# Kernel optimization log

Measured on AMD Instinct MI355X. Metric: run time of the kernel, lower is better.

The kernel has to match this reference:

```python
import jax, jax.numpy as jnp
from jax import lax
import numpy as np

L = 6            # layer_number
CHEB2 = 4        # chebyshev_number ** 2
C = 4 * CHEB2    # per-block channel size = 16
G = 2 ** L       # final block grid = 64 (freq_len / leftover)


def _pool_avg2(y):
    # AvgPool2d kernel=2 stride=2 (dims always divisible here)
    B, Ch, H, W = y.shape
    return y.reshape(B, Ch, H // 2, 2, W // 2, 2).mean(axis=(3, 5))


def _wrap_pad1(y):
    # period_padding by 1 on bottom/right (circular)
    return jnp.pad(y, ((0, 0), (0, 0), (0, 1), (0, 1)), mode='wrap')


def _conv(x, w, groups=1):
    return lax.conv_general_dilated(x, w, (1, 1), 'VALID', feature_group_count=groups)


def _forward(x, W0, b0, Wr, br, Wft, bft):
    B = x.shape[0]
    z0 = jnp.zeros_like(x)
    # split: real input -> (Re+, Re-, Im+=0, Im-=0) per channel (in_channel=1)
    y = jnp.concatenate([jax.nn.relu(x), jax.nn.relu(-x), z0, z0], axis=1)  # [B,4,64,64]
    # layer 0: kernel (w_h,w_w)=(2,2), 4 -> 4*4*cheb^2 = 64
    y = _conv(y, W0) + b0[None, :, None, None]  # [B,64,63,63]
    y = jax.nn.relu(y)
    y = _pool_avg2(_wrap_pad1(y))               # [B,64,32,32] = 2^(L-1) grid
    # recursion layers: per-block 2x2 conv C -> 4C, batched as grouped conv
    for lyr in range(1, L):
        g = 2 ** lyr
        nb = g * g
        z = _conv(y, Wr[lyr - 1], groups=nb) + br[lyr - 1][None, :, None, None]
        s = z.shape[-1]                          # 2^(L-lyr) - 1
        # grouped-conv channel order [A_y, A_x, y_loc, x_loc, C] ->
        # target block index 2^(lyr+1)*(2*A_y+y_loc) + (2*A_x+x_loc):
        z = z.reshape(B, g, g, 2, 2, C, s, s).transpose(0, 1, 3, 2, 4, 5, 6, 7)
        z = z.reshape(B, nb * 4 * C, s, s)
        z = jax.nn.relu(z)
        y = _pool_avg2(_wrap_pad1(z))            # spatial halves -> 2^(L-lyr-1)
    # FT layer: 4^L blocks, 1x1 conv C -> 4*leftover^2 = 4, spatial is 1x1
    v = y.reshape(B, G * G, C)
    f = jnp.einsum('bnc,noc->bno', v, Wft) + bft[None]  # [B,4096,4]
    f = f.reshape(B, G, G, 4)                            # (ky, kx) frequency grid
    real = f[..., 0] - f[..., 1]
    imag = f[..., 2] - f[..., 3]
    return jnp.stack([real, imag], axis=1)               # [B,2,64,64]


def setup_inputs() -> dict:
    key = jax.random.key(0)
    ks = jax.random.split(key, 16)
    sc = 0.1
    inp = {
        'x':  jax.random.normal(ks[0], (256, 1, 64, 64), jnp.float32),
        'W0': sc * jax.random.normal(ks[1], (64, 4, 2, 2), jnp.float32),
        'b0': sc * jax.random.normal(ks[2], (64,), jnp.float32),
        'Wft': sc * jax.random.normal(ks[3], (4096, 4, 16), jnp.float32),
        'bft': sc * jax.random.normal(ks[4], (4096, 4), jnp.float32),
    }
    for lyr in range(1, L):
        nb = 4 ** lyr
        inp[f'W{lyr}'] = sc * jax.random.normal(ks[4 + 2 * lyr - 1], (nb * 4 * C, C, 2, 2), jnp.float32)
        inp[f'b{lyr}'] = sc * jax.random.normal(ks[4 + 2 * lyr], (nb * 4 * C,), jnp.float32)
    return inp


def reference(x, W0, b0, W1, b1, W2, b2, W3, b3, W4, b4, W5, b5, Wft, bft):
    Wr = (W1, W2, W3, W4, W5)
    br = (b1, b2, b3, b4, b5)
    return _forward(x, W0, b0, Wr, br, Wft, bft)
```

## Files before the change

kernel.cpp:

```cpp
#include <hip/hip_runtime.h>
#include <hip/hip_bf16.h>


typedef __attribute__((ext_vector_type(4))) float f32x4;
typedef __attribute__((ext_vector_type(8))) short s16x8;

__device__ __forceinline__ short f2bf(float f) {
  union { float f; unsigned u; } v; v.f = f;
  unsigned r = v.u + 0x7fff + ((v.u >> 16) & 1);
  return (short)(r >> 16);
}
__device__ __forceinline__ float bf2f(short s) {
  union { unsigned u; float f; } v; v.u = ((unsigned)(unsigned short)s) << 16;
  return v.f;
}
constexpr int ilog2c(int v) { return v <= 1 ? 0 : 1 + ilog2c(v / 2); }

__global__ __launch_bounds__(256) void k_layer0(
    const float* __restrict__ x, const float* __restrict__ W0,
    const float* __restrict__ b0, short* __restrict__ out) {
  constexpr int GS = 4112;
  __shared__ __align__(16) float xs[17 * 64];
  __shared__ __align__(16) short os[4 * GS];
  const int b = blockIdx.x, p0 = blockIdx.y * 8;
  const float* xb = x + (size_t)b * 4096;
  for (int i = threadIdx.x; i < 17 * 16; i += 256) {
    int lr = i >> 4, c4 = i & 15;
    ((float4*)xs)[i] = *(const float4*)(xb + ((2 * p0 + lr) & 63) * 64 + c4 * 4);
  }
  __syncthreads();
  const int oc = threadIdx.x & 63, wv = threadIdx.x >> 6;
  const int g = oc >> 4, c = oc & 15;
  float wp[2][2], wm[2][2];
#pragma unroll
  for (int kh = 0; kh < 2; ++kh)
#pragma unroll
    for (int kw = 0; kw < 2; ++kw) {
      wp[kh][kw] = W0[((oc * 4 + 0) * 2 + kh) * 2 + kw];
      wm[kh][kw] = W0[((oc * 4 + 1) * 2 + kh) * 2 + kw];
    }
  const float bias = b0[oc];
  for (int t = wv; t < 64; t += 4) {
    const int phl = t >> 3, c0 = (t & 7) * 8;
    const int lrA = 2 * phl;
    float vA[9], vB[9], vC[9];
#pragma unroll
    for (int j = 0; j < 8; ++j) {
      vA[j] = xs[lrA * 64 + c0 + j];
      vB[j] = xs[(lrA + 1) * 64 + c0 + j];
      vC[j] = xs[(lrA + 2) * 64 + c0 + j];
    }
    vA[8] = xs[lrA * 64 + ((c0 + 8) & 63)];
    vB[8] = xs[(lrA + 1) * 64 + ((c0 + 8) & 63)];
    vC[8] = xs[(lrA + 2) * 64 + ((c0 + 8) & 63)];
    float pA[9], mA[9], pB[9], mB[9], pC[9], mC[9];
#pragma unroll
    for (int j = 0; j < 9; ++j) {
      pA[j] = fmaxf(vA[j], 0.f); mA[j] = pA[j] - vA[j];
      pB[j] = fmaxf(vB[j], 0.f); mB[j] = pB[j] - vB[j];
      pC[j] = fmaxf(vC[j], 0.f); mC[j] = pC[j] - vC[j];
    }
    float sc0[8], sc1[8];
#pragma unroll
    for (int q = 0; q < 8; ++q) {
      sc0[q] = bias + wp[0][0] * pA[q] + wm[0][0] * mA[q] + wp[0][1] * pA[q + 1] + wm[0][1] * mA[q + 1]
                    + wp[1][0] * pB[q] + wm[1][0] * mB[q] + wp[1][1] * pB[q + 1] + wm[1][1] * mB[q + 1];
      sc1[q] = bias + wp[0][0] * pB[q] + wm[0][0] * mB[q] + wp[0][1] * pB[q + 1] + wm[0][1] * mB[q + 1]
                    + wp[1][0] * pC[q] + wm[1][0] * mC[q] + wp[1][1] * pC[q + 1] + wm[1][1] * mC[q + 1];
    }
#pragma unroll
    for (int p = 0; p < 4; ++p) {
      float po = 0.25f * (fmaxf(sc0[2 * p], 0.f) + fmaxf(sc0[2 * p + 1], 0.f) +
                          fmaxf(sc1[2 * p], 0.f) + fmaxf(sc1[2 * p + 1], 0.f));
      os[g * GS + (phl * 32 + c0 / 2 + p) * 16 + c] = f2bf(po);
    }
  }
  __syncthreads();
#pragma unroll
  for (int gg = 0; gg < 4; ++gg) {
    short* dst = out + ((size_t)b * 4 + gg) * 16384 + (size_t)p0 * 512;
    for (int i = threadIdx.x; i < 512; i += 256)
      *(float4*)&dst[i * 8] = *(const float4*)&os[gg * GS + i * 8];
  }
}

template <int S, int G, int IMB, int PH>
__global__ __launch_bounds__(256) void k_bconv(
    const short* __restrict__ yin, const float* __restrict__ W,
    const float* __restrict__ Bv, short* __restrict__ yout) {
  constexpr int NB = G * G;
  constexpr int SO = S / 2;
  constexpr int LOG_SO = ilog2c(SO);
  constexpr int LOG_PH = ilog2c(PH);
  constexpr int SP = S + 1;
  constexpr int ROWS = 2 * PH + 1;
  constexpr int IMG_PIX = ROWS * SP;
  constexpr int ITERS = IMB * PH * SO / 64;
  __shared__ __align__(16) short ins[IMB * IMG_PIX * 16];
  __shared__ __align__(16) short wl[4096];
  const int gi = blockIdx.y;
  const int b0 = blockIdx.x * IMB;
  const int p0 = blockIdx.z * PH;
  const int tid = threadIdx.x;

  const float* wsrc = W + (size_t)gi * 4096;
  for (int i = tid; i < 4096; i += 256) {
    int j = i & 7, row = (i >> 3) & 15, g = (i >> 7) & 3, dy = (i >> 9) & 1, t = i >> 10;
    int k = 8 * g + j;
    int ic = k & 15, dx = k >> 4;
    wl[i] = f2bf(wsrc[((t * 16 + row) * 16 + ic) * 4 + dy * 2 + dx]);
  }
  constexpr int GRAN = IMB * IMG_PIX * 2;
  for (int i = tid; i < GRAN; i += 256) {
    int half = i & 1, q = i >> 1;
    int xx = q % SP; int t2 = q / SP; int lr = t2 % ROWS; int bi2 = t2 / ROWS;
    int gr = (2 * p0 + lr) & (S - 1);
    int gx = xx & (S - 1);
    size_t src = (((size_t)(b0 + bi2) * NB + gi) * (S * S) + gr * S + gx) * 16 + half * 8;
    *(float4*)&ins[(size_t)q * 16 + half * 8] = *(const float4*)&yin[src];
  }
  __syncthreads();

  const int lane = tid & 63, wv = tid >> 6;
  const int lp = lane & 15, g4 = lane >> 4;
  const int dxg = g4 >> 1, ich = g4 & 1;

  s16x8 af[4][2];
#pragma unroll
  for (int t = 0; t < 4; ++t)
#pragma unroll
    for (int dy = 0; dy < 2; ++dy)
      af[t][dy] = *(const s16x8*)&wl[(((t * 2 + dy) * 4 + g4) * 16 + lp) * 8];
  f32x4 bv[4];
#pragma unroll
  for (int t = 0; t < 4; ++t)
    bv[t] = *(const f32x4*)&Bv[(size_t)gi * 64 + t * 16 + g4 * 4];

  const int A_y = gi / G, A_x = gi - A_y * G;

#pragma unroll
  for (int it = 0; it < ITERS; ++it) {
    const int pg = it * 64 + wv * 16 + lp;
    const int px = pg & (SO - 1);
    const int pyl = (pg >> LOG_SO) & (PH - 1);
    const int bi = pg >> (LOG_SO + LOG_PH);
    const int py = p0 + pyl;
    const short* pb = ins + ((size_t)(bi * ROWS + 2 * pyl) * SP + 2 * px + dxg) * 16 + ich * 8;
    const short* r0 = pb;
    const short* r1 = pb + SP * 16;
    const short* r2 = pb + 2 * SP * 16;
    f32x4 acc[4][4];
#pragma unroll
    for (int t = 0; t < 4; ++t)
#pragma unroll
      for (int ph = 0; ph < 4; ++ph) acc[t][ph] = bv[t];
#pragma unroll
    for (int phy = 0; phy < 2; ++phy)
#pragma unroll
      for (int phx = 0; phx < 2; ++phx) {
        const int ph = phy * 2 + phx;
#pragma unroll
        for (int dy = 0; dy < 2; ++dy) {
          const short* rp = (phy + dy == 0) ? r0 : (phy + dy == 1) ? r1 : r2;
          s16x8 bf = *(const s16x8*)(rp + phx * 16);
#pragma unroll
          for (int t = 0; t < 4; ++t)
            acc[t][ph] = __builtin_amdgcn_mfma_f32_16x16x32_bf16(af[t][dy], bf, acc[t][ph], 0, 0, 0);
        }
      }
    const int b = b0 + bi;
#pragma unroll
    for (int t = 0; t < 4; ++t) {
      short pk[4];
#pragma unroll
      for (int r = 0; r < 4; ++r) {
        float po = 0.25f * (fmaxf(acc[t][0][r], 0.f) + fmaxf(acc[t][1][r], 0.f) +
                            fmaxf(acc[t][2][r], 0.f) + fmaxf(acc[t][3][r], 0.f));
        pk[r] = f2bf(po);
      }
      const int gip = (A_y * 2 + (t >> 1)) * (2 * G) + A_x * 2 + (t & 1);
      size_t dst = (((size_t)b * (4 * NB) + gip) * (SO * SO) + py * SO + px) * 16 + g4 * 4;
      *(short4*)&yout[dst] = make_short4(pk[0], pk[1], pk[2], pk[3]);
    }
  }
}

__global__ __launch_bounds__(256) void k_ft(
    const short* __restrict__ v, const float* __restrict__ Wft,
    const float* __restrict__ bft, float* __restrict__ out) {
  const int n = blockIdx.x * 64 + (threadIdx.x & 63);
  const int b0 = blockIdx.y * 32 + (threadIdx.x >> 6) * 8;
  float w[64];
  const float4* wp = (const float4*)(Wft + (size_t)n * 64);
#pragma unroll
  for (int j = 0; j < 16; ++j) {
    float4 t = wp[j];
    w[4 * j] = t.x; w[4 * j + 1] = t.y; w[4 * j + 2] = t.z; w[4 * j + 3] = t.w;
  }
  const float4 bq = *(const float4*)(bft + (size_t)n * 4);
#pragma unroll 2
  for (int bb = 0; bb < 8; ++bb) {
    const int b = b0 + bb;
    const short* vp = v + ((size_t)b * 4096 + n) * 16;
    s16x8 a0 = *(const s16x8*)vp;
    s16x8 a1 = *(const s16x8*)(vp + 8);
    float vv[16];
#pragma unroll
    for (int j = 0; j < 8; ++j) { vv[j] = bf2f(a0[j]); vv[8 + j] = bf2f(a1[j]); }
    float f0 = bq.x, f1 = bq.y, f2 = bq.z, f3 = bq.w;
#pragma unroll
    for (int j = 0; j < 16; ++j) {
      f0 += vv[j] * w[j];
      f1 += vv[j] * w[16 + j];
      f2 += vv[j] * w[32 + j];
      f3 += vv[j] * w[48 + j];
    }
    out[(size_t)b * 8192 + n] = f0 - f1;
    out[(size_t)b * 8192 + 4096 + n] = f2 - f3;
  }
}

extern "C" void kernel_launch(void* const* d_in, const int* in_sizes, int n_in,
                              void* d_out, int out_size, void* d_ws, size_t ws_size,
                              hipStream_t stream) {
  const float* x   = (const float*)d_in[0];
  const float* W0  = (const float*)d_in[1];
  const float* b0  = (const float*)d_in[2];
  const float* Wft = (const float*)d_in[3];
  const float* bft = (const float*)d_in[4];
  const float* W1 = (const float*)d_in[5];  const float* b1 = (const float*)d_in[6];
  const float* W2 = (const float*)d_in[7];  const float* b2 = (const float*)d_in[8];
  const float* W3 = (const float*)d_in[9];  const float* b3 = (const float*)d_in[10];
  const float* W4 = (const float*)d_in[11]; const float* b4 = (const float*)d_in[12];
  const float* W5 = (const float*)d_in[13]; const float* b5 = (const float*)d_in[14];

  short* buf0 = (short*)d_ws;
  short* buf1 = buf0 + (size_t)16777216;

  k_layer0<<<dim3(256, 4), 256, 0, stream>>>(x, W0, b0, buf0);
  k_bconv<32, 2, 1, 4><<<dim3(256, 4, 4), 256, 0, stream>>>(buf0, W1, b1, buf1);
  k_bconv<16, 4, 4, 4><<<dim3(64, 16, 2), 256, 0, stream>>>(buf1, W2, b2, buf0);
  k_bconv<8, 8, 8, 4><<<dim3(32, 64, 1), 256, 0, stream>>>(buf0, W3, b3, buf1);
  k_bconv<4, 16, 32, 2><<<dim3(8, 256, 1), 256, 0, stream>>>(buf1, W4, b4, buf0);
  k_bconv<2, 32, 128, 1><<<dim3(2, 1024, 1), 256, 0, stream>>>(buf0, W5, b5, buf1);
  k_ft<<<dim3(64, 8), 256, 0, stream>>>(buf1, Wft, bft, (float*)d_out);
}
```

Measured before the change: 269.5 us.

## Pre-convert block weights to bf16 once and read conv inputs directly from global

Adds a kernel that converts all recursion-layer weights to bf16 in MFMA fragment order in one pass, so each block-conv workgroup no longer converts 4096 floats on entry. The block-conv kernels drop the LDS input staging and syncthreads and load their B fragments straight from global memory per wave, with a new grid mapping of a fixed number of 16-pixel chunks per wave. This trades LDS reuse of overlapping 3x2 input windows for redundant global/L2 reads, and adds an extra launch plus workspace for the bf16 weights.

```diff
diff --git a/kernel.cpp b/kernel.cpp
--- a/kernel.cpp
+++ b/kernel.cpp
@@ -15,6 +15,32 @@
   return v.f;
 }
 constexpr int ilog2c(int v) { return v <= 1 ? 0 : 1 + ilog2c(v / 2); }
+
+#define WOFF1 0
+#define WOFF2 16384
+#define WOFF3 81920
+#define WOFF4 344064
+#define WOFF5 1392640
+#define WTOT  5586944
+
+__global__ __launch_bounds__(256) void k_wconv(
+    const float* __restrict__ W1, const float* __restrict__ W2,
+    const float* __restrict__ W3, const float* __restrict__ W4,
+    const float* __restrict__ W5, short* __restrict__ wbf) {
+  const int idx = blockIdx.x * 256 + threadIdx.x;
+  if (idx >= WTOT) return;
+  const float* src;
+  int local;
+  if (idx < WOFF2)      { src = W1; local = idx; }
+  else if (idx < WOFF3) { src = W2; local = idx - WOFF2; }
+  else if (idx < WOFF4) { src = W3; local = idx - WOFF3; }
+  else if (idx < WOFF5) { src = W4; local = idx - WOFF4; }
+  else                  { src = W5; local = idx - WOFF5; }
+  const int gi = local >> 12, i = local & 4095;
+  const int j = i & 7, row = (i >> 3) & 15, g = (i >> 7) & 3, dy = (i >> 9) & 1, t = i >> 10;
+  const int k = 8 * g + j, ic = k & 15, dx = k >> 4;
+  wbf[idx] = f2bf(src[(size_t)gi * 4096 + ((t * 16 + row) * 16 + ic) * 4 + dy * 2 + dx]);
+}
 
 __global__ __launch_bounds__(256) void k_layer0(
     const float* __restrict__ x, const float* __restrict__ W0,
@@ -84,47 +110,19 @@
   }
 }
 
-template <int S, int G, int IMB, int PH>
+template <int S, int G, int ITW>
 __global__ __launch_bounds__(256) void k_bconv(
-    const short* __restrict__ yin, const float* __restrict__ W,
+    const short* __restrict__ yin, const short* __restrict__ wbf,
     const float* __restrict__ Bv, short* __restrict__ yout) {
   constexpr int NB = G * G;
   constexpr int SO = S / 2;
   constexpr int LOG_SO = ilog2c(SO);
-  constexpr int LOG_PH = ilog2c(PH);
-  constexpr int SP = S + 1;
-  constexpr int ROWS = 2 * PH + 1;
-  constexpr int IMG_PIX = ROWS * SP;
-  constexpr int ITERS = IMB * PH * SO / 64;
-  __shared__ __align__(16) short ins[IMB * IMG_PIX * 16];
-  __shared__ __align__(16) short wl[4096];
   const int gi = blockIdx.y;
-  const int b0 = blockIdx.x * IMB;
-  const int p0 = blockIdx.z * PH;
-  const int tid = threadIdx.x;
-
-  const float* wsrc = W + (size_t)gi * 4096;
-  for (int i = tid; i < 4096; i += 256) {
-    int j = i & 7, row = (i >> 3) & 15, g = (i >> 7) & 3, dy = (i >> 9) & 1, t = i >> 10;
-    int k = 8 * g + j;
-    int ic = k & 15, dx = k >> 4;
-    wl[i] = f2bf(wsrc[((t * 16 + row) * 16 + ic) * 4 + dy * 2 + dx]);
-  }
-  constexpr int GRAN = IMB * IMG_PIX * 2;
-  for (int i = tid; i < GRAN; i += 256) {
-    int half = i & 1, q = i >> 1;
-    int xx = q % SP; int t2 = q / SP; int lr = t2 % ROWS; int bi2 = t2 / ROWS;
-    int gr = (2 * p0 + lr) & (S - 1);
-    int gx = xx & (S - 1);
-    size_t src = (((size_t)(b0 + bi2) * NB + gi) * (S * S) + gr * S + gx) * 16 + half * 8;
-    *(float4*)&ins[(size_t)q * 16 + half * 8] = *(const float4*)&yin[src];
-  }
-  __syncthreads();
-
-  const int lane = tid & 63, wv = tid >> 6;
+  const int lane = threadIdx.x & 63, wv = threadIdx.x >> 6;
   const int lp = lane & 15, g4 = lane >> 4;
   const int dxg = g4 >> 1, ich = g4 & 1;
 
+  const short* wl = wbf + (size_t)gi * 4096;
   s16x8 af[4][2];
 #pragma unroll
   for (int t = 0; t < 4; ++t)
@@ -137,18 +135,25 @@
     bv[t] = *(const f32x4*)&Bv[(size_t)gi * 64 + t * 16 + g4 * 4];
 
   const int A_y = gi / G, A_x = gi - A_y * G;
-
-#pragma unroll
-  for (int it = 0; it < ITERS; ++it) {
-    const int pg = it * 64 + wv * 16 + lp;
+  const int chunk0 = (blockIdx.x * 4 + wv) * ITW;
+
+#pragma unroll
+  for (int it = 0; it < ITW; ++it) {
+    const int pg = (chunk0 + it) * 16 + lp;
     const int px = pg & (SO - 1);
-    const int pyl = (pg >> LOG_SO) & (PH - 1);
-    const int bi = pg >> (LOG_SO + LOG_PH);
-    const int py = p0 + pyl;
-    const short* pb = ins + ((size_t)(bi * ROWS + 2 * pyl) * SP + 2 * px + dxg) * 16 + ich * 8;
-    const short* r0 = pb;
-    const short* r1 = pb + SP * 16;
-    const short* r2 = pb + 2 * SP * 16;
+    const int py = (pg >> LOG_SO) & (SO - 1);
+    const int bi = pg >> (2 * LOG_SO);
+    const size_t base = ((size_t)bi * NB + gi) * (S * S * 16) + ich * 8;
+    s16x8 bf[3][2];
+#pragma unroll
+    for (int rr = 0; rr < 3; ++rr) {
+      const int r = (2 * py + rr) & (S - 1);
+#pragma unroll
+      for (int cc = 0; cc < 2; ++cc) {
+        const int c = (2 * px + dxg + cc) & (S - 1);
+        bf[rr][cc] = *(const s16x8*)&yin[base + (size_t)(r * S + c) * 16];
+      }
+    }
     f32x4 acc[4][4];
 #pragma unroll
     for (int t = 0; t < 4; ++t)
@@ -161,14 +166,12 @@
         const int ph = phy * 2 + phx;
 #pragma unroll
         for (int dy = 0; dy < 2; ++dy) {
-          const short* rp = (phy + dy == 0) ? r0 : (phy + dy == 1) ? r1 : r2;
-          s16x8 bf = *(const s16x8*)(rp + phx * 16);
+          s16x8 frag = bf[phy + dy][phx];
 #pragma unroll
           for (int t = 0; t < 4; ++t)
-            acc[t][ph] = __builtin_amdgcn_mfma_f32_16x16x32_bf16(af[t][dy], bf, acc[t][ph], 0, 0, 0);
+            acc[t][ph] = __builtin_amdgcn_mfma_f32_16x16x32_bf16(af[t][dy], frag, acc[t][ph], 0, 0, 0);
         }
       }
-    const int b = b0 + bi;
 #pragma unroll
     for (int t = 0; t < 4; ++t) {
       short pk[4];
@@ -179,7 +182,7 @@
         pk[r] = f2bf(po);
       }
       const int gip = (A_y * 2 + (t >> 1)) * (2 * G) + A_x * 2 + (t & 1);
-      size_t dst = (((size_t)b * (4 * NB) + gip) * (SO * SO) + py * SO + px) * 16 + g4 * 4;
+      size_t dst = (((size_t)bi * (4 * NB) + gip) * (SO * SO) + py * SO + px) * 16 + g4 * 4;
       *(short4*)&yout[dst] = make_short4(pk[0], pk[1], pk[2], pk[3]);
     }
   }
@@ -236,12 +239,14 @@
 
   short* buf0 = (short*)d_ws;
   short* buf1 = buf0 + (size_t)16777216;
-
+  short* wbf  = buf1 + (size_t)16777216;
+
+  k_wconv<<<(WTOT + 255) / 256, 256, 0, stream>>>(W1, W2, W3, W4, W5, wbf);
   k_layer0<<<dim3(256, 4), 256, 0, stream>>>(x, W0, b0, buf0);
-  k_bconv<32, 2, 1, 4><<<dim3(256, 4, 4), 256, 0, stream>>>(buf0, W1, b1, buf1);
-  k_bconv<16, 4, 4, 4><<<dim3(64, 16, 2), 256, 0, stream>>>(buf1, W2, b2, buf0);
-  k_bconv<8, 8, 8, 4><<<dim3(32, 64, 1), 256, 0, stream>>>(buf0, W3, b3, buf1);
-  k_bconv<4, 16, 32, 2><<<dim3(8, 256, 1), 256, 0, stream>>>(buf1, W4, b4, buf0);
-  k_bconv<2, 32, 128, 1><<<dim3(2, 1024, 1), 256, 0, stream>>>(buf0, W5, b5, buf1);
+  k_bconv<32, 2, 2><<<dim3(512, 4), 256, 0, stream>>>(buf0, wbf + WOFF1, b1, buf1);
+  k_bconv<16, 4, 2><<<dim3(128, 16), 256, 0, stream>>>(buf1, wbf + WOFF2, b2, buf0);
+  k_bconv<8, 8, 2><<<dim3(32, 64), 256, 0, stream>>>(buf0, wbf + WOFF3, b3, buf1);
+  k_bconv<4, 16, 2><<<dim3(8, 256), 256, 0, stream>>>(buf1, wbf + WOFF4, b4, buf0);
+  k_bconv<2, 32, 2><<<dim3(2, 1024), 256, 0, stream>>>(buf0, wbf + WOFF5, b5, buf1);
   k_ft<<<dim3(64, 8), 256, 0, stream>>>(buf1, Wft, bft, (float*)d_out);
 }
```

Result: faster. 233.4 us (-13.4%).
